# Kernel optimization log

Hardware: AMD Instinct MI355X
Metric: run time of the kernel (lower is better)

## Reference

```python
import jax, jax.numpy as jnp
import numpy as np

# Static config (matches init_kwargs / docstring example)
SHAPES = ((100, 100), (50, 50), (25, 25), (13, 13))  # (H, W) per level
L, P, NH, HD, E, F = 4, 4, 8, 32, 256, 1024
NUM_LAYERS = 6
EPS = 1e-5
NUM_KEYS = sum(h * w for h, w in SHAPES)  # 13294


def _ln(x, g, b):
    m = jnp.mean(x, -1, keepdims=True)
    v = jnp.var(x, -1, keepdims=True)
    return (x - m) * jax.lax.rsqrt(v + EPS) * g + b


def _ms_deform_attn(value, loc, aw):
    # value: (B,N,NH,HD)  loc: (B,N,NH,L,P,2) normalized  aw: (B,N,NH,L,P)
    B, N = value.shape[:2]
    out = jnp.zeros((B, NH, N, HD), value.dtype)
    start = 0
    for lvl, (h, w) in enumerate(SHAPES):
        v = value[:, start:start + h * w].transpose(0, 2, 1, 3)  # (B,NH,hw,HD)
        start += h * w
        # grid_sample align_corners=False pixel coords
        x = loc[:, :, :, lvl, :, 0] * w - 0.5  # (B,N,NH,P)
        y = loc[:, :, :, lvl, :, 1] * h - 0.5
        x0 = jnp.floor(x); y0 = jnp.floor(y)
        lx = x - x0; ly = y - y0
        x0 = x0.astype(jnp.int32); y0 = y0.astype(jnp.int32)

        def gather(yi, xi):
            valid = ((xi >= 0) & (xi < w) & (yi >= 0) & (yi < h)).astype(value.dtype)
            idx = jnp.clip(yi, 0, h - 1) * w + jnp.clip(xi, 0, w - 1)  # (B,N,NH,P)
            idx = idx.transpose(0, 2, 1, 3).reshape(B, NH, N * P, 1)
            got = jnp.take_along_axis(v, idx, axis=2).reshape(B, NH, N, P, HD)
            return got * valid.transpose(0, 2, 1, 3)[..., None]

        def wgt(a):  # (B,N,NH,P) -> (B,NH,N,P,1)
            return a.transpose(0, 2, 1, 3)[..., None]

        samp = (gather(y0, x0) * wgt((1 - lx) * (1 - ly))
                + gather(y0, x0 + 1) * wgt(lx * (1 - ly))
                + gather(y0 + 1, x0) * wgt((1 - lx) * ly)
                + gather(y0 + 1, x0 + 1) * wgt(lx * ly))  # (B,NH,N,P,HD)
        out = out + jnp.sum(samp * wgt(aw[:, :, :, lvl]), axis=3)
    return out.transpose(0, 2, 1, 3).reshape(B, N, NH * HD)


def _layer(x, ref, Woff, boff, Waw, baw, Wv, bv, Wo, bo, ln1_g, ln1_b, Wf1, bf1, Wf2, bf2, ln2_g, ln2_b):
    B, N, _ = x.shape
    v = (x @ Wv + bv).reshape(B, N, NH, HD)
    off = (x @ Woff + boff).reshape(B, N, NH, L, P, 2)
    aw = jax.nn.softmax((x @ Waw + baw).reshape(B, N, NH, L * P), -1).reshape(B, N, NH, L, P)
    normalizer = jnp.asarray([[w, h] for (h, w) in SHAPES], x.dtype)  # (L,2) in (x,y)=(W,H)
    loc = ref[:, :, None, :, None, :] + off / normalizer[None, None, None, :, None, :]
    attn = _ms_deform_attn(v, loc, aw) @ Wo + bo
    x = _ln(x + attn, ln1_g, ln1_b)
    f = jax.nn.relu(x @ Wf1 + bf1) @ Wf2 + bf2
    return _ln(x + f, ln2_g, ln2_b)


def setup_inputs() -> dict:
    key = jax.random.key(0)
    ks = jax.random.split(key, 10)
    s = 0.02
    return {
        "src": jax.random.normal(ks[0], (2, NUM_KEYS, E), jnp.float32),
        "reference_points": jax.random.uniform(ks[1], (2, NUM_KEYS, L, 2), jnp.float32),
        "spatial_shapes": jnp.asarray(SHAPES, jnp.int32),
        "level_start_index": jnp.asarray([0, 10000, 12500, 13125], jnp.int32),
        "Woff": jax.random.normal(ks[2], (E, NH * L * P * 2), jnp.float32) * s,
        "boff": jnp.zeros((NH * L * P * 2,), jnp.float32),
        "Waw": jax.random.normal(ks[3], (E, NH * L * P), jnp.float32) * s,
        "baw": jnp.zeros((NH * L * P,), jnp.float32),
        "Wv": jax.random.normal(ks[4], (E, E), jnp.float32) * s,
        "bv": jnp.zeros((E,), jnp.float32),
        "Wo": jax.random.normal(ks[5], (E, E), jnp.float32) * s,
        "bo": jnp.zeros((E,), jnp.float32),
        "ln1_g": jnp.ones((E,), jnp.float32),
        "ln1_b": jnp.zeros((E,), jnp.float32),
        "Wf1": jax.random.normal(ks[6], (E, F), jnp.float32) * s,
        "bf1": jnp.zeros((F,), jnp.float32),
        "Wf2": jax.random.normal(ks[7], (F, E), jnp.float32) * s,
        "bf2": jnp.zeros((E,), jnp.float32),
        "ln2_g": jnp.ones((E,), jnp.float32),
        "ln2_b": jnp.zeros((E,), jnp.float32),
    }


def reference(src, reference_points, spatial_shapes, level_start_index, Woff, boff, Waw, baw, Wv, bv, Wo, bo, ln1_g, ln1_b, Wf1, bf1, Wf2, bf2, ln2_g, ln2_b):
    # NOTE: the torch encoder reuses the SAME layer object num_layers times,
    # so parameters are shared across all 6 layers.
    x = src
    for _ in range(NUM_LAYERS):
        x = _layer(x, reference_points, Woff, boff, Waw, baw, Wv, bv, Wo, bo,
                   ln1_g, ln1_b, Wf1, bf1, Wf2, bf2, ln2_g, ln2_b)
    return x
```

## Files before the change

### kernel.cpp

```cpp
#include <hip/hip_runtime.h>
#include <hip/hip_bf16.h>
#include <math.h>

#define NKEYS 13294
#define BATCH 2
#define MROWS (BATCH * NKEYS)
#define EDIM  256
#define FDIM  1024
#define EPSV  1e-5f

typedef __bf16 bf16x8 __attribute__((ext_vector_type(8)));
typedef float  f32x4  __attribute__((ext_vector_type(4)));

__device__ __forceinline__ void async16(const void* g, void* l) {
    __builtin_amdgcn_global_load_lds(
        (const __attribute__((address_space(1))) void*)g,
        (__attribute__((address_space(3))) void*)l, 16, 0, 0);
}

template<int MODE>
__global__ __launch_bounds__(256, 4) void gemm_mfma_k(
    const __hip_bfloat16* __restrict__ A, const __hip_bfloat16* __restrict__ WT,
    const float* __restrict__ bias, __hip_bfloat16* __restrict__ Cout,
    int M, int N, int K,
    __hip_bfloat16* __restrict__ o_vb, __hip_bfloat16* __restrict__ o_off,
    __hip_bfloat16* __restrict__ o_aw)
{
    constexpr int BM = 64, BN = 128, BKc = 32;
    constexpr int SM = (BM + BN) * BKc;
    __shared__ __hip_bfloat16 smem[2 * SM];

    const int tid  = threadIdx.x;
    const int bm   = blockIdx.y * BM;
    const int bn   = blockIdx.x * BN;
    const int lane = tid & 63;
    const int w    = tid >> 6;
    const int wr   = w >> 1, wc = w & 1;
    const int l15  = lane & 15, quad = lane >> 4;

    int arow = bm + (tid >> 2); if (arow >= M) arow = M - 1;
    const int kc8 = (tid & 3) * 8;
    const __hip_bfloat16* gA  = A  + (size_t)arow * K + kc8;
    const __hip_bfloat16* gB0 = WT + (size_t)(bn + (tid >> 2)) * K + kc8;
    const __hip_bfloat16* gB1 = WT + (size_t)(bn + 64 + (tid >> 2)) * K + kc8;
    const int oA  = tid * 8;
    const int oB0 = BM * BKc + tid * 8;
    const int oB1 = BM * BKc + 64 * BKc + tid * 8;

    f32x4 acc[2][4];
    #pragma unroll
    for (int i = 0; i < 2; ++i)
        #pragma unroll
        for (int j = 0; j < 4; ++j) acc[i][j] = (f32x4)0.f;

    const int T = K / BKc;
    async16(gA,  smem + oA);
    async16(gB0, smem + oB0);
    async16(gB1, smem + oB1);

    for (int it = 0; it < T; ++it) {
        __syncthreads();
        if (it + 1 < T) {
            const int nxt = ((it + 1) & 1) * SM;
            const int ko  = (it + 1) * BKc;
            async16(gA  + ko, smem + nxt + oA);
            async16(gB0 + ko, smem + nxt + oB0);
            async16(gB1 + ko, smem + nxt + oB1);
        }
        const __hip_bfloat16* sA = smem + (it & 1) * SM;
        const __hip_bfloat16* sB = sA + BM * BKc;

        bf16x8 a[2], b[4];
        #pragma unroll
        for (int mt = 0; mt < 2; ++mt)
            a[mt] = *(const bf16x8*)&sA[(wr * 32 + mt * 16 + l15) * BKc + quad * 8];
        #pragma unroll
        for (int nt = 0; nt < 4; ++nt)
            b[nt] = *(const bf16x8*)&sB[(wc * 64 + nt * 16 + l15) * BKc + quad * 8];
        #pragma unroll
        for (int mt = 0; mt < 2; ++mt)
            #pragma unroll
            for (int nt = 0; nt < 4; ++nt)
                acc[mt][nt] = __builtin_amdgcn_mfma_f32_16x16x32_bf16(
                    a[mt], b[nt], acc[mt][nt], 0, 0, 0);
    }

    #pragma unroll
    for (int mt = 0; mt < 2; ++mt) {
        #pragma unroll
        for (int nt = 0; nt < 4; ++nt) {
            const int col = bn + wc * 64 + nt * 16 + l15;
            const float bz = bias[col];
            #pragma unroll
            for (int r = 0; r < 4; ++r) {
                const int row = bm + wr * 32 + mt * 16 + quad * 4 + r;
                if (row >= M) continue;
                float vv = acc[mt][nt][r] + bz;
                if (MODE == 1) {
                    if (col < 256) {
                        const int b = (row >= NKEYS) ? 1 : 0;
                        const int h = col >> 5, d = col & 31;
                        o_vb[((size_t)(b * 7 + h) * NKEYS + row) * 32 + d] = __float2bfloat16(vv);
                    } else if (col < 512) {
                        o_off[(size_t)row * 256 + (col - 256)] = __float2bfloat16(vv);
                    } else {
                        o_aw[(size_t)row * 128 + (col - 512)] = __float2bfloat16(vv);
                    }
                } else {
                    if (MODE == 3) vv = fmaxf(vv, 0.f);
                    Cout[(size_t)row * N + col] = __float2bfloat16(vv);
                }
            }
        }
    }
}

__global__ __launch_bounds__(256, 4) void gemm_ln_k(
    const __hip_bfloat16* __restrict__ A, const __hip_bfloat16* __restrict__ WT,
    const float* __restrict__ bias, const float* __restrict__ xres,
    const float* __restrict__ g, const float* __restrict__ bta,
    float* __restrict__ xout, __hip_bfloat16* __restrict__ xbout,
    int M, int K)
{
    constexpr int BM = 32, BN = 256, BKc = 32;
    constexpr int ROWS = BM + BN;
    constexpr int SM = ROWS * BKc;
    __shared__ __hip_bfloat16 smem[2 * SM];

    const int tid  = threadIdx.x;
    const int bm   = blockIdx.x * BM;
    const int lane = tid & 63;
    const int w    = tid >> 6;
    const int l15  = lane & 15, quad = lane >> 4;

    const int gRow = tid >> 2;
    const int kc8  = (tid & 3) * 8;
    const __hip_bfloat16* gsrc[5];
    int ldsoff[5];
    bool vmask[5];
    #pragma unroll
    for (int rr = 0; rr < 5; ++rr) {
        int grow = gRow + 64 * rr;
        vmask[rr] = (grow < ROWS);
        int gr = vmask[rr] ? grow : 0;
        if (gr < BM) {
            int ar = bm + gr; if (ar >= M) ar = M - 1;
            gsrc[rr] = A + (size_t)ar * K + kc8;
        } else {
            gsrc[rr] = WT + (size_t)(gr - BM) * K + kc8;
        }
        ldsoff[rr] = gr * BKc + kc8;
    }

    f32x4 acc[2][4];
    #pragma unroll
    for (int i = 0; i < 2; ++i)
        #pragma unroll
        for (int j = 0; j < 4; ++j) acc[i][j] = (f32x4)0.f;

    const int T = K / BKc;
    #pragma unroll
    for (int rr = 0; rr < 5; ++rr)
        if (vmask[rr]) async16(gsrc[rr], smem + ldsoff[rr]);

    for (int it = 0; it < T; ++it) {
        __syncthreads();
        if (it + 1 < T) {
            const int nxt = ((it + 1) & 1) * SM;
            const int ko  = (it + 1) * BKc;
            #pragma unroll
            for (int rr = 0; rr < 5; ++rr)
                if (vmask[rr]) async16(gsrc[rr] + ko, smem + nxt + ldsoff[rr]);
        }
        const __hip_bfloat16* sA = smem + (it & 1) * SM;
        const __hip_bfloat16* sB = sA + BM * BKc;

        bf16x8 a[2], b[4];
        #pragma unroll
        for (int mt = 0; mt < 2; ++mt)
            a[mt] = *(const bf16x8*)&sA[(mt * 16 + l15) * BKc + quad * 8];
        #pragma unroll
        for (int nt = 0; nt < 4; ++nt)
            b[nt] = *(const bf16x8*)&sB[(w * 64 + nt * 16 + l15) * BKc + quad * 8];
        #pragma unroll
        for (int mt = 0; mt < 2; ++mt)
            #pragma unroll
            for (int nt = 0; nt < 4; ++nt)
                acc[mt][nt] = __builtin_amdgcn_mfma_f32_16x16x32_bf16(
                    a[mt], b[nt], acc[mt][nt], 0, 0, 0);
    }

    const int colb = w * 64;
    float bz[4], gz[4], bb[4];
    #pragma unroll
    for (int nt = 0; nt < 4; ++nt) {
        const int col = colb + nt * 16 + l15;
        bz[nt] = bias[col]; gz[nt] = g[col]; bb[nt] = bta[col];
    }
    #pragma unroll
    for (int mt = 0; mt < 2; ++mt)
        #pragma unroll
        for (int r = 0; r < 4; ++r) {
            int row = bm + mt * 16 + quad * 4 + r;
            if (row >= M) row = M - 1;
            #pragma unroll
            for (int nt = 0; nt < 4; ++nt)
                acc[mt][nt][r] += bz[nt] + xres[(size_t)row * 256 + colb + nt * 16 + l15];
        }

    __syncthreads();
    float* stats = (float*)smem;
    #pragma unroll
    for (int mt = 0; mt < 2; ++mt)
        #pragma unroll
        for (int r = 0; r < 4; ++r) {
            float s = 0.f, sq = 0.f;
            #pragma unroll
            for (int nt = 0; nt < 4; ++nt) {
                const float v = acc[mt][nt][r];
                s += v; sq += v * v;
            }
            #pragma unroll
            for (int m = 1; m < 16; m <<= 1) {
                s  += __shfl_xor(s,  m, 64);
                sq += __shfl_xor(sq, m, 64);
            }
            if (l15 == 0) {
                const int rl = mt * 16 + quad * 4 + r;
                stats[(w * 32 + rl) * 2 + 0] = s;
                stats[(w * 32 + rl) * 2 + 1] = sq;
            }
        }
    __syncthreads();

    #pragma unroll
    for (int mt = 0; mt < 2; ++mt)
        #pragma unroll
        for (int r = 0; r < 4; ++r) {
            const int rl  = mt * 16 + quad * 4 + r;
            const int row = bm + rl;
            float s  = stats[rl * 2]     + stats[(32 + rl) * 2]
                     + stats[(64 + rl) * 2] + stats[(96 + rl) * 2];
            float sq = stats[rl * 2 + 1] + stats[(32 + rl) * 2 + 1]
                     + stats[(64 + rl) * 2 + 1] + stats[(96 + rl) * 2 + 1];
            const float mean = s * (1.f / 256.f);
            const float var  = sq * (1.f / 256.f) - mean * mean;
            const float rstd = rsqrtf(var + EPSV);
            if (row < M) {
                #pragma unroll
                for (int nt = 0; nt < 4; ++nt) {
                    const int col = colb + nt * 16 + l15;
                    const float v = (acc[mt][nt][r] - mean) * rstd * gz[nt] + bb[nt];
                    xout[(size_t)row * 256 + col]  = v;
                    xbout[(size_t)row * 256 + col] = __float2bfloat16(v);
                }
            }
        }
}

__global__ void convert_wt_k(const float* __restrict__ W, __hip_bfloat16* __restrict__ WT,
                             int K, int N, int rowOff)
{
    const int idx = blockIdx.x * 256 + threadIdx.x;
    if (idx >= K * N) return;
    const int k = idx / N, n = idx % N;
    WT[(size_t)(rowOff + n) * K + k] = __float2bfloat16(W[idx]);
}

__global__ void pack_bias_k(const float* __restrict__ bv, const float* __restrict__ boff,
                            const float* __restrict__ baw, float* __restrict__ dst)
{
    const int i = blockIdx.x * 256 + threadIdx.x;
    if (i < 256) dst[i] = bv[i];
    else if (i < 512) dst[i] = boff[i - 256];
    else if (i < 640) dst[i] = baw[i - 512];
}

__global__ void convert_src_k(const float* __restrict__ src, float* __restrict__ x,
                              __hip_bfloat16* __restrict__ xb)
{
    const int i = blockIdx.x * 256 + threadIdx.x;
    const float4 v = ((const float4*)src)[i];
    ((float4*)x)[i] = v;
    xb[i * 4 + 0] = __float2bfloat16(v.x);
    xb[i * 4 + 1] = __float2bfloat16(v.y);
    xb[i * 4 + 2] = __float2bfloat16(v.z);
    xb[i * 4 + 3] = __float2bfloat16(v.w);
}

__global__ __launch_bounds__(256) void sample_k(
    const __hip_bfloat16* __restrict__ v_bf,
    const __hip_bfloat16* __restrict__ offb,
    const __hip_bfloat16* __restrict__ awb,
    const float* __restrict__ ref,
    __hip_bfloat16* __restrict__ out)
{
    __shared__ alignas(16) float sw[272][4];
    __shared__ alignas(16) int   sa[272][4];
    const int t  = threadIdx.x;
    const int q0 = blockIdx.x * 2;
    const int qi = t >> 7, h = (t >> 4) & 7;

    {
        const int i = t & 15;
        const int q = q0 + qi;
        const int l = i >> 2;
        const float logit = __bfloat162float(awb[(size_t)q * 128 + h * 16 + i]);
        float mx = logit;
        #pragma unroll
        for (int m = 1; m < 16; m <<= 1) mx = fmaxf(mx, __shfl_xor(mx, m, 64));
        const float e = __expf(logit - mx);
        float s = e;
        #pragma unroll
        for (int m = 1; m < 16; m <<= 1) s += __shfl_xor(s, m, 64);
        const float aw = e / s;

        const int ww = (l == 0) ? 100 : (l == 1) ? 50 : (l == 2) ? 25 : 13;
        const int ls = (l == 0) ? 0 : (l == 1) ? 10000 : (l == 2) ? 12500 : 13125;
        const int b  = (q >= NKEYS) ? 1 : 0;
        const int slab = (b * 8 + h) * NKEYS + ls;

        const __hip_bfloat162 ofp = *(const __hip_bfloat162*)&offb[(size_t)q * 256 + h * 32 + i * 2];
        const float2 rf = *(const float2*)&ref[(size_t)q * 8 + l * 2];
        const float x = rf.x * (float)ww + __bfloat162float(ofp.x) - 0.5f;
        const float y = rf.y * (float)ww + __bfloat162float(ofp.y) - 0.5f;
        const float x0f = floorf(x), y0f = floorf(y);
        const float lx = x - x0f, ly = y - y0f;
        const int x0 = (int)x0f, y0 = (int)y0f;
        const bool x0ok = (x0 >= 0) & (x0 < ww);
        const bool x1ok = (x0 + 1 >= 0) & (x0 + 1 < ww);
        const bool y0ok = (y0 >= 0) & (y0 < ww);
        const bool y1ok = (y0 + 1 >= 0) & (y0 + 1 < ww);

        float w00 = (1.f - lx) * (1.f - ly) * aw;
        float w01 = lx * (1.f - ly) * aw;
        float w10 = (1.f - lx) * ly * aw;
        float w11 = lx * ly * aw;
        int a00 = slab + y0 * ww + x0;
        int a01 = a00 + 1;
        int a10 = a00 + ww;
        int a11 = a10 + 1;
        if (!(y0ok & x0ok)) { w00 = 0.f; a00 = 0; }
        if (!(y0ok & x1ok)) { w01 = 0.f; a01 = 0; }
        if (!(y1ok & x0ok)) { w10 = 0.f; a10 = 0; }
        if (!(y1ok & x1ok)) { w11 = 0.f; a11 = 0; }

        const int idx = (qi * 8 + h) * 17 + i;
        sw[idx][0] = w00; sw[idx][1] = w01; sw[idx][2] = w10; sw[idx][3] = w11;
        sa[idx][0] = a00 * 64; sa[idx][1] = a01 * 64;
        sa[idx][2] = a10 * 64; sa[idx][3] = a11 * 64;
    }
    __syncthreads();

    const int d2 = t & 15;
    const unsigned d4 = d2 * 4;
    const char* vb = (const char*)v_bf;
    const int ebase = (qi * 8 + h) * 17;
    float acc0 = 0.f, acc1 = 0.f;
    #pragma unroll
    for (int i = 0; i < 16; ++i) {
        const f32x4 wv = *(const f32x4*)sw[ebase + i];
        const int4  av = *(const int4*)sa[ebase + i];
        const unsigned p0 = *(const unsigned*)(vb + ((unsigned)av.x + d4));
        const unsigned p1 = *(const unsigned*)(vb + ((unsigned)av.y + d4));
        const unsigned p2 = *(const unsigned*)(vb + ((unsigned)av.z + d4));
        const unsigned p3 = *(const unsigned*)(vb + ((unsigned)av.w + d4));
        acc0 += wv[0] * __uint_as_float(p0 << 16);
        acc1 += wv[0] * __uint_as_float(p0 & 0xffff0000u);
        acc0 += wv[1] * __uint_as_float(p1 << 16);
        acc1 += wv[1] * __uint_as_float(p1 & 0xffff0000u);
        acc0 += wv[2] * __uint_as_float(p2 << 16);
        acc1 += wv[2] * __uint_as_float(p2 & 0xffff0000u);
        acc0 += wv[3] * __uint_as_float(p3 << 16);
        acc1 += wv[3] * __uint_as_float(p3 & 0xffff0000u);
    }
    __hip_bfloat162 ov;
    ov.x = __float2bfloat16(acc0);
    ov.y = __float2bfloat16(acc1);
    *(__hip_bfloat162*)&out[(size_t)(q0 + qi) * 256 + h * 32 + d2 * 2] = ov;
}

extern "C" void kernel_launch(void* const* d_in, const int* in_sizes, int n_in,
                              void* d_out, int out_size, void* d_ws, size_t ws_size,
                              hipStream_t stream)
{
    const float* src  = (const float*)d_in[0];
    const float* ref  = (const float*)d_in[1];
    const float* Woff = (const float*)d_in[4];
    const float* boff = (const float*)d_in[5];
    const float* Waw  = (const float*)d_in[6];
    const float* baw  = (const float*)d_in[7];
    const float* Wv   = (const float*)d_in[8];
    const float* bv   = (const float*)d_in[9];
    const float* Wo   = (const float*)d_in[10];
    const float* bo   = (const float*)d_in[11];
    const float* ln1g = (const float*)d_in[12];
    const float* ln1b = (const float*)d_in[13];
    const float* Wf1  = (const float*)d_in[14];
    const float* bf1  = (const float*)d_in[15];
    const float* Wf2  = (const float*)d_in[16];
    const float* bf2  = (const float*)d_in[17];
    const float* ln2g = (const float*)d_in[18];
    const float* ln2b = (const float*)d_in[19];

    float* x = (float*)d_out;

    float* ws = (float*)d_ws;
    float* bias1 = ws;
    __hip_bfloat16* v_bf  = (__hip_bfloat16*)(bias1 + 640);
    __hip_bfloat16* offb  = v_bf  + (size_t)MROWS * 256;
    __hip_bfloat16* awb   = offb  + (size_t)MROWS * 256;
    __hip_bfloat16* xb    = awb   + (size_t)MROWS * 128;
    __hip_bfloat16* attnb = xb    + (size_t)MROWS * 256;
    __hip_bfloat16* hb    = attnb + (size_t)MROWS * 256;
    __hip_bfloat16* WT1   = hb    + (size_t)MROWS * 1024;
    __hip_bfloat16* WTo   = WT1   + 640 * 256;
    __hip_bfloat16* WTf1  = WTo   + 256 * 256;
    __hip_bfloat16* WTf2  = WTf1  + 1024 * 256;

    convert_wt_k<<<(256 * 256 + 255) / 256, 256, 0, stream>>>(Wv,   WT1,  256, 256,   0);
    convert_wt_k<<<(256 * 256 + 255) / 256, 256, 0, stream>>>(Woff, WT1,  256, 256, 256);
    convert_wt_k<<<(256 * 128 + 255) / 256, 256, 0, stream>>>(Waw,  WT1,  256, 128, 512);
    convert_wt_k<<<(256 * 256 + 255) / 256, 256, 0, stream>>>(Wo,   WTo,  256, 256,   0);
    convert_wt_k<<<(256 * 1024 + 255) / 256, 256, 0, stream>>>(Wf1, WTf1, 256, 1024,  0);
    convert_wt_k<<<(1024 * 256 + 255) / 256, 256, 0, stream>>>(Wf2, WTf2, 1024, 256,  0);
    pack_bias_k<<<3, 256, 0, stream>>>(bv, boff, baw, bias1);
    convert_src_k<<<(MROWS * 64 + 255) / 256, 256, 0, stream>>>(src, x, xb);

    const int gy  = (MROWS + 63) / 64;
    const int gln = (MROWS + 31) / 32;
    for (int layer = 0; layer < 6; ++layer) {
        gemm_mfma_k<1><<<dim3(640 / 128, gy), 256, 0, stream>>>(
            xb, WT1, bias1, nullptr, MROWS, 640, 256, v_bf, offb, awb);
        sample_k<<<MROWS / 2, 256, 0, stream>>>(v_bf, offb, awb, ref, attnb);
        gemm_ln_k<<<gln, 256, 0, stream>>>(
            attnb, WTo, bo, x, ln1g, ln1b, x, xb, MROWS, 256);
        gemm_mfma_k<3><<<dim3(1024 / 128, gy), 256, 0, stream>>>(
            xb, WTf1, bf1, hb, MROWS, 1024, 256, nullptr, nullptr, nullptr);
        gemm_ln_k<<<gln, 256, 0, stream>>>(
            hb, WTf2, bf2, x, ln2g, ln2b, x, xb, MROWS, 1024);
    }
}
```

Baseline: 1.191 ms.

## Triple-buffer GEMM pipelines and keep residual stream in bf16 only

```diff
diff --git a/kernel.cpp b/kernel.cpp
--- a/kernel.cpp
+++ b/kernel.cpp
@@ -17,6 +17,8 @@
         (const __attribute__((address_space(1))) void*)g,
         (__attribute__((address_space(3))) void*)l, 16, 0, 0);
 }
+#define WAITVM(n) __builtin_amdgcn_s_waitcnt(0x0F70 | (n))
+#define RAWBAR()  __builtin_amdgcn_s_barrier()
 
 template<int MODE>
 __global__ __launch_bounds__(256, 4) void gemm_mfma_k(
@@ -27,8 +29,8 @@
     __hip_bfloat16* __restrict__ o_aw)
 {
     constexpr int BM = 64, BN = 128, BKc = 32;
-    constexpr int SM = (BM + BN) * BKc;
-    __shared__ __hip_bfloat16 smem[2 * SM];
+    constexpr int SMX = (BM + BN) * BKc;
+    __shared__ __hip_bfloat16 smem[3 * SMX];
 
     const int tid  = threadIdx.x;
     const int bm   = blockIdx.y * BM;
@@ -54,20 +56,21 @@
         for (int j = 0; j < 4; ++j) acc[i][j] = (f32x4)0.f;
 
     const int T = K / BKc;
-    async16(gA,  smem + oA);
-    async16(gB0, smem + oB0);
-    async16(gB1, smem + oB1);
-
+    #pragma unroll
+    for (int s = 0; s < 3; ++s) {
+        const int ko = s * BKc;
+        async16(gA  + ko, smem + s * SMX + oA);
+        async16(gB0 + ko, smem + s * SMX + oB0);
+        async16(gB1 + ko, smem + s * SMX + oB1);
+    }
+
+    int cons = 0;
     for (int it = 0; it < T; ++it) {
-        __syncthreads();
-        if (it + 1 < T) {
-            const int nxt = ((it + 1) & 1) * SM;
-            const int ko  = (it + 1) * BKc;
-            async16(gA  + ko, smem + nxt + oA);
-            async16(gB0 + ko, smem + nxt + oB0);
-            async16(gB1 + ko, smem + nxt + oB1);
-        }
-        const __hip_bfloat16* sA = smem + (it & 1) * SM;
+        if (it + 2 < T)      WAITVM(6);
+        else if (it + 1 < T) WAITVM(3);
+        else                 WAITVM(0);
+        RAWBAR();
+        const __hip_bfloat16* sA = smem + cons * SMX;
         const __hip_bfloat16* sB = sA + BM * BKc;
 
         bf16x8 a[2], b[4];
@@ -83,6 +86,14 @@
             for (int nt = 0; nt < 4; ++nt)
                 acc[mt][nt] = __builtin_amdgcn_mfma_f32_16x16x32_bf16(
                     a[mt], b[nt], acc[mt][nt], 0, 0, 0);
+        RAWBAR();
+        if (it + 3 < T) {
+            const int ko = (it + 3) * BKc;
+            async16(gA  + ko, smem + cons * SMX + oA);
+            async16(gB0 + ko, smem + cons * SMX + oB0);
+            async16(gB1 + ko, smem + cons * SMX + oB1);
+        }
+        cons = (cons == 2) ? 0 : cons + 1;
     }
 
     #pragma unroll
@@ -115,17 +126,18 @@
     }
 }
 
-__global__ __launch_bounds__(256, 4) void gemm_ln_k(
+template<int FINAL>
+__global__ __launch_bounds__(256, 2) void gemm_ln_k(
     const __hip_bfloat16* __restrict__ A, const __hip_bfloat16* __restrict__ WT,
-    const float* __restrict__ bias, const float* __restrict__ xres,
+    const float* __restrict__ bias, const __hip_bfloat16* __restrict__ xres,
     const float* __restrict__ g, const float* __restrict__ bta,
-    float* __restrict__ xout, __hip_bfloat16* __restrict__ xbout,
+    float* __restrict__ xfout, __hip_bfloat16* __restrict__ xbout,
     int M, int K)
 {
     constexpr int BM = 32, BN = 256, BKc = 32;
-    constexpr int ROWS = BM + BN;
-    constexpr int SM = ROWS * BKc;
-    __shared__ __hip_bfloat16 smem[2 * SM];
+    constexpr int ROWS = 320;
+    constexpr int SMX = ROWS * BKc;
+    __shared__ __hip_bfloat16 smem[3 * SMX];
 
     const int tid  = threadIdx.x;
     const int bm   = blockIdx.x * BM;
@@ -137,17 +149,15 @@
     const int kc8  = (tid & 3) * 8;
     const __hip_bfloat16* gsrc[5];
     int ldsoff[5];
-    bool vmask[5];
     #pragma unroll
     for (int rr = 0; rr < 5; ++rr) {
-        int grow = gRow + 64 * rr;
-        vmask[rr] = (grow < ROWS);
-        int gr = vmask[rr] ? grow : 0;
+        const int gr = gRow + 64 * rr;
         if (gr < BM) {
             int ar = bm + gr; if (ar >= M) ar = M - 1;
             gsrc[rr] = A + (size_t)ar * K + kc8;
         } else {
-            gsrc[rr] = WT + (size_t)(gr - BM) * K + kc8;
+            int br = gr - BM; if (br > 255) br = 255;
+            gsrc[rr] = WT + (size_t)br * K + kc8;
         }
         ldsoff[rr] = gr * BKc + kc8;
     }
@@ -160,19 +170,20 @@
 
     const int T = K / BKc;
     #pragma unroll
-    for (int rr = 0; rr < 5; ++rr)
-        if (vmask[rr]) async16(gsrc[rr], smem + ldsoff[rr]);
-
+    for (int s = 0; s < 3; ++s) {
+        const int ko = s * BKc;
+        #pragma unroll
+        for (int rr = 0; rr < 5; ++rr)
+            async16(gsrc[rr] + ko, smem + s * SMX + ldsoff[rr]);
+    }
+
+    int cons = 0;
     for (int it = 0; it < T; ++it) {
-        __syncthreads();
-        if (it + 1 < T) {
-            const int nxt = ((it + 1) & 1) * SM;
-            const int ko  = (it + 1) * BKc;
-            #pragma unroll
-            for (int rr = 0; rr < 5; ++rr)
-                if (vmask[rr]) async16(gsrc[rr] + ko, smem + nxt + ldsoff[rr]);
-        }
-        const __hip_bfloat16* sA = smem + (it & 1) * SM;
+        if (it + 2 < T)      WAITVM(10);
+        else if (it + 1 < T) WAITVM(5);
+        else                 WAITVM(0);
+        RAWBAR();
+        const __hip_bfloat16* sA = smem + cons * SMX;
         const __hip_bfloat16* sB = sA + BM * BKc;
 
         bf16x8 a[2], b[4];
@@ -188,6 +199,14 @@
             for (int nt = 0; nt < 4; ++nt)
                 acc[mt][nt] = __builtin_amdgcn_mfma_f32_16x16x32_bf16(
                     a[mt], b[nt], acc[mt][nt], 0, 0, 0);
+        RAWBAR();
+        if (it + 3 < T) {
+            const int ko = (it + 3) * BKc;
+            #pragma unroll
+            for (int rr = 0; rr < 5; ++rr)
+                async16(gsrc[rr] + ko, smem + cons * SMX + ldsoff[rr]);
+        }
+        cons = (cons == 2) ? 0 : cons + 1;
     }
 
     const int colb = w * 64;
@@ -205,7 +224,8 @@
             if (row >= M) row = M - 1;
             #pragma unroll
             for (int nt = 0; nt < 4; ++nt)
-                acc[mt][nt][r] += bz[nt] + xres[(size_t)row * 256 + colb + nt * 16 + l15];
+                acc[mt][nt][r] += bz[nt] + __bfloat162float(
+                    xres[(size_t)row * 256 + colb + nt * 16 + l15]);
         }
 
     __syncthreads();
@@ -239,9 +259,9 @@
         for (int r = 0; r < 4; ++r) {
             const int rl  = mt * 16 + quad * 4 + r;
             const int row = bm + rl;
-            float s  = stats[rl * 2]     + stats[(32 + rl) * 2]
-                     + stats[(64 + rl) * 2] + stats[(96 + rl) * 2];
-            float sq = stats[rl * 2 + 1] + stats[(32 + rl) * 2 + 1]
+            float s  = stats[rl * 2]         + stats[(32 + rl) * 2]
+                     + stats[(64 + rl) * 2]  + stats[(96 + rl) * 2];
+            float sq = stats[rl * 2 + 1]     + stats[(32 + rl) * 2 + 1]
                      + stats[(64 + rl) * 2 + 1] + stats[(96 + rl) * 2 + 1];
             const float mean = s * (1.f / 256.f);
             const float var  = sq * (1.f / 256.f) - mean * mean;
@@ -251,8 +271,8 @@
                 for (int nt = 0; nt < 4; ++nt) {
                     const int col = colb + nt * 16 + l15;
                     const float v = (acc[mt][nt][r] - mean) * rstd * gz[nt] + bb[nt];
-                    xout[(size_t)row * 256 + col]  = v;
                     xbout[(size_t)row * 256 + col] = __float2bfloat16(v);
+                    if (FINAL) xfout[(size_t)row * 256 + col] = v;
                 }
             }
         }
@@ -276,12 +296,10 @@
     else if (i < 640) dst[i] = baw[i - 512];
 }
 
-__global__ void convert_src_k(const float* __restrict__ src, float* __restrict__ x,
-                              __hip_bfloat16* __restrict__ xb)
+__global__ void convert_src_k(const float* __restrict__ src, __hip_bfloat16* __restrict__ xb)
 {
     const int i = blockIdx.x * 256 + threadIdx.x;
     const float4 v = ((const float4*)src)[i];
-    ((float4*)x)[i] = v;
     xb[i * 4 + 0] = __float2bfloat16(v.x);
     xb[i * 4 + 1] = __float2bfloat16(v.y);
     xb[i * 4 + 2] = __float2bfloat16(v.z);
@@ -425,7 +443,7 @@
     convert_wt_k<<<(256 * 1024 + 255) / 256, 256, 0, stream>>>(Wf1, WTf1, 256, 1024,  0);
     convert_wt_k<<<(1024 * 256 + 255) / 256, 256, 0, stream>>>(Wf2, WTf2, 1024, 256,  0);
     pack_bias_k<<<3, 256, 0, stream>>>(bv, boff, baw, bias1);
-    convert_src_k<<<(MROWS * 64 + 255) / 256, 256, 0, stream>>>(src, x, xb);
+    convert_src_k<<<(MROWS * 64 + 255) / 256, 256, 0, stream>>>(src, xb);
 
     const int gy  = (MROWS + 63) / 64;
     const int gln = (MROWS + 31) / 32;
@@ -433,11 +451,15 @@
         gemm_mfma_k<1><<<dim3(640 / 128, gy), 256, 0, stream>>>(
             xb, WT1, bias1, nullptr, MROWS, 640, 256, v_bf, offb, awb);
         sample_k<<<MROWS / 2, 256, 0, stream>>>(v_bf, offb, awb, ref, attnb);
-        gemm_ln_k<<<gln, 256, 0, stream>>>(
-            attnb, WTo, bo, x, ln1g, ln1b, x, xb, MROWS, 256);
+        gemm_ln_k<0><<<gln, 256, 0, stream>>>(
+            attnb, WTo, bo, xb, ln1g, ln1b, nullptr, xb, MROWS, 256);
         gemm_mfma_k<3><<<dim3(1024 / 128, gy), 256, 0, stream>>>(
             xb, WTf1, bf1, hb, MROWS, 1024, 256, nullptr, nullptr, nullptr);
-        gemm_ln_k<<<gln, 256, 0, stream>>>(
-            hb, WTf2, bf2, x, ln2g, ln2b, x, xb, MROWS, 1024);
-    }
-}
+        if (layer < 5)
+            gemm_ln_k<0><<<gln, 256, 0, stream>>>(
+                hb, WTf2, bf2, xb, ln2g, ln2b, nullptr, xb, MROWS, 1024);
+        else
+            gemm_ln_k<1><<<gln, 256, 0, stream>>>(
+                hb, WTf2, bf2, xb, ln2g, ln2b, x, xb, MROWS, 1024);
+    }
+}
```

Measured after the change: 1.251 ms. 5.1% more time.
